# Kernel optimization log

Hardware: AMD Instinct MI355X
Metric: run time of the kernel (lower is better)

Reference implementation:

```python
import jax, jax.numpy as jnp
import numpy as np
from jax import lax

# --- STE quantizers matching the torch autograd.Functions ---
@jax.custom_vjp
def binary_quantize_w(x):
    return jnp.sign(x)

def _bqw_fwd(x):
    return jnp.sign(x), None

def _bqw_bwd(_, g):
    return (g,)  # straight-through identity

binary_quantize_w.defvjp(_bqw_fwd, _bqw_bwd)

@jax.custom_vjp
def binary_quantize_a(x):
    return jnp.sign(x)

def _bqa_fwd(x):
    return jnp.sign(x), x

def _bqa_bwd(x, g):
    return (jnp.clip(2.0 - jnp.abs(2.0 * x), a_min=0.0) * g,)

binary_quantize_a.defvjp(_bqa_fwd, _bqa_bwd)

STRIDE = 1
PAD = 1

def setup_inputs() -> dict:
    key = jax.random.key(0)
    k1, k2, k3 = jax.random.split(key, 3)
    x = jax.random.normal(k1, (32, 256, 56, 56), dtype=jnp.float32)
    M = jax.random.normal(k2, (256, 256, 3, 3), dtype=jnp.float32)
    Alpha = jax.random.uniform(k3, (256, 1, 1), dtype=jnp.float32)
    return {"x": x, "M": M, "Alpha": Alpha}

def reference(x, M, Alpha):
    bw = binary_quantize_w(M)        # (O, I, kh, kw), +/-1
    ba = binary_quantize_a(x)        # (N, C, H, W), +/-1
    out = lax.conv_general_dilated(
        ba, bw,
        window_strides=(STRIDE, STRIDE),
        padding=[(PAD, PAD), (PAD, PAD)],
        dimension_numbers=("NCHW", "OIHW", "NCHW"),
    )
    # Alpha (O,1,1) broadcasts over (N, O, H, W) trailing dims -> per-channel scale
    return out * Alpha
```

## Files before the change

kernel.cpp:

```cpp
#include <hip/hip_runtime.h>
#include <stdint.h>


typedef __attribute__((ext_vector_type(16))) float floatx16;
typedef __attribute__((ext_vector_type(8)))  int   intx8;

#define N_IMG 32
#define C_IN  256
#define O_OUT 256
#define HP 58
#define WP 58
#define GPI 3136
#define APAD_POS ((size_t)N_IMG * HP * WP)
#define APAD_BYTES (APAD_POS * C_IN)
#define TPI 13
#define AL_GRAN 1072
#define WL_GRAN 1536

__device__ __forceinline__ unsigned int sgn8(float x) {
    return x > 0.f ? 0x38u : (x < 0.f ? 0xB8u : 0u);
}

__device__ __forceinline__ void glds16(const unsigned char* g, unsigned char* l) {
    __builtin_amdgcn_global_load_lds(
        (const __attribute__((address_space(1))) unsigned int*)g,
        (__attribute__((address_space(3))) unsigned int*)l, 16, 0, 0);
}

__global__ __launch_bounds__(256) void binarize_act(
    const float* __restrict__ x, unsigned char* __restrict__ apad)
{
    int bid = blockIdx.x;
    int n = bid / HP;
    int hp = bid - n * HP;
    int tid = threadIdx.x;

    unsigned char* rowp = apad + ((size_t)(n * HP + hp) * WP) * C_IN;
    uint4 z = {0u, 0u, 0u, 0u};

    if (hp == 0 || hp == HP - 1) {
#pragma unroll
        for (int j = 0; j < 4; ++j) {
            int t = tid + 256 * j;
            if (t < WP * 16) {
                int w = t >> 4, g = t & 15;
                *(uint4*)(rowp + (size_t)w * C_IN + g * 16) = z;
            }
        }
        return;
    }
    int h = hp - 1;

    __shared__ unsigned int tile[C_IN * 15];
    __shared__ unsigned int lds2[56 * 65];

    const float* xb = x + ((size_t)n * C_IN) * GPI + h * 56;
#pragma unroll
    for (int j = 0; j < 14; ++j) {
        int t = tid + 256 * j;
        int ci = t / 14;
        int w4 = t - ci * 14;
        float4 v = *(const float4*)(xb + (size_t)ci * GPI + w4 * 4);
        tile[ci * 15 + w4] = sgn8(v.x) | (sgn8(v.y) << 8) |
                             (sgn8(v.z) << 16) | (sgn8(v.w) << 24);
    }
    __syncthreads();

#pragma unroll
    for (int j = 0; j < 14; ++j) {
        int t = tid + 256 * j;
        int wlo = t & 3;
        int cq  = (t >> 2) & 63;
        int whi = t >> 8;
        int sh = wlo * 8;
        unsigned int r = 0;
#pragma unroll
        for (int i = 0; i < 4; ++i) {
            unsigned int v = tile[(cq * 4 + i) * 15 + whi];
            r |= ((v >> sh) & 0xFFu) << (8 * i);
        }
        lds2[(whi * 4 + wlo) * 65 + cq] = r;
    }
    __syncthreads();

#pragma unroll
    for (int j = 0; j < 4; ++j) {
        int t = tid + 256 * j;
        if (t < 896) {
            int w = t >> 4, g = t & 15;
            uint4 v;
            v.x = lds2[w * 65 + g * 4 + 0];
            v.y = lds2[w * 65 + g * 4 + 1];
            v.z = lds2[w * 65 + g * 4 + 2];
            v.w = lds2[w * 65 + g * 4 + 3];
            *(uint4*)(rowp + (size_t)(w + 1) * C_IN + g * 16) = v;
        }
    }
    if (tid < 32) {
        int g = tid & 15;
        int col = (tid >> 4) * (WP - 1);
        *(uint4*)(rowp + (size_t)col * C_IN + g * 16) = z;
    }
}

__global__ __launch_bounds__(256) void pack_w(
    const float* __restrict__ M, unsigned char* __restrict__ wpk)
{
    int gid = blockIdx.x * 256 + threadIdx.x;
    int o = gid >> 6;
    int c4 = (gid & 63) << 2;
    const float* mb = M + (size_t)(o * C_IN + c4) * 9;
#pragma unroll
    for (int t = 0; t < 9; ++t) {
        unsigned int r = sgn8(mb[t]) | (sgn8(mb[9 + t]) << 8) |
                         (sgn8(mb[18 + t]) << 16) | (sgn8(mb[27 + t]) << 24);
        *(unsigned int*)(wpk + (size_t)t * 65536 + o * C_IN + c4) = r;
    }
}

__global__ __launch_bounds__(256, 2) void bconv_gemm(
    const unsigned char* __restrict__ apad,
    const unsigned char* __restrict__ wpk,
    const float* __restrict__ alpha,
    float* __restrict__ out)
{
    __shared__ __align__(16) unsigned char Al[AL_GRAN * 16];
    __shared__ __align__(16) unsigned char Wl[WL_GRAN * 16];

    const int tid = threadIdx.x;
    const int wv = tid >> 6, lane = tid & 63;
    const int l31 = lane & 31, hb = lane >> 5;

    const int bid = blockIdx.x;
    const int img = bid / 26;
    const int rem = bid - img * 26;
    const int tl = rem >> 1, ot = rem & 1;
    const int g0 = tl << 8;
    const int h0 = g0 / 56, w0 = g0 - h0 * 56;
    const int o_base = ot << 7;
    const int Q0 = (img * HP + h0) * WP + w0;

    int al_pos[5], al_sl[5];
#pragma unroll
    for (int it = 0; it < 5; ++it) {
        int s = (it < 4) ? (tid + (it << 8)) : (tid + 816);
        int pos = s >> 2, gI = s & 3;
        al_pos[it] = pos;
        al_sl[it]  = ((gI - (pos >> 1)) & 3) << 4;
    }
    int wl_off[6];
#pragma unroll
    for (int it = 0; it < 6; ++it) {
        int s = tid + (it << 8);
        int r = s >> 2, gI = s & 3;
        int kw = r >> 7, o = r & 127;
        int sl = (gI - (r >> 1)) & 3;
        wl_off[it] = kw * 65536 + o * 256 + (sl << 4);
    }

    const int o_half  = (wv >> 1) << 6;
    const int px_half = (wv & 1) << 7;

    int pos_tab[4], pxg[4];
#pragma unroll
    for (int nt = 0; nt < 4; ++nt) {
        int px = px_half + (nt << 5) + l31;
        pxg[nt] = g0 + px;
        int pxc = (pxg[nt] < GPI) ? px : (GPI - 1 - g0);
        pos_tab[nt] = pxc + 2 * ((w0 + pxc) / 56);
    }

    floatx16 acc[2][4] = {};

    for (int kh = 0; kh < 3; ++kh) {
        const int rowbase = Q0 + kh * WP;
        const int plim = (int)APAD_POS - 1 - rowbase;
        const unsigned char* asrc0 = apad + ((size_t)rowbase << 8);
        const unsigned char* wsrc0 = wpk + (size_t)(kh * 3) * 65536 + ((size_t)o_base << 8);
        for (int c0 = 0; c0 < C_IN; c0 += 64) {
            const unsigned char* asrc = asrc0 + c0;
            const unsigned char* wsrc = wsrc0 + c0;
            __syncthreads();
#pragma unroll
            for (int it = 0; it < 4; ++it) {
                int p = al_pos[it] < plim ? al_pos[it] : plim;
                glds16(asrc + ((size_t)p << 8) + al_sl[it],
                       &Al[(size_t)((it << 8) + (wv << 6)) << 4]);
            }
            {
                int p = al_pos[4] < plim ? al_pos[4] : plim;
                glds16(asrc + ((size_t)p << 8) + al_sl[4],
                       &Al[(size_t)(816 + (wv << 6)) << 4]);
            }
#pragma unroll
            for (int it = 0; it < 6; ++it)
                glds16(wsrc + wl_off[it],
                       &Wl[(size_t)((it << 8) + (wv << 6)) << 4]);
            __syncthreads();

#pragma unroll
            for (int kw = 0; kw < 3; ++kw) {
                union F { long l[4]; intx8 v; };
                F af[2];
#pragma unroll
                for (int mt = 0; mt < 2; ++mt) {
                    int r = (kw << 7) + o_half + (mt << 5) + l31;
#pragma unroll
                    for (int ks = 0; ks < 4; ++ks) {
                        int g = (r << 2) + ((ks + (r >> 1)) & 3);
                        af[mt].l[ks] = *(const long*)&Wl[(size_t)(g << 4) + (hb << 3)];
                    }
                }
#pragma unroll
                for (int nt = 0; nt < 4; ++nt) {
                    int pos = pos_tab[nt] + kw;
                    F bf;
#pragma unroll
                    for (int ks = 0; ks < 4; ++ks) {
                        int g = (pos << 2) + ((ks + (pos >> 1)) & 3);
                        bf.l[ks] = *(const long*)&Al[(size_t)(g << 4) + (hb << 3)];
                    }
#pragma unroll
                    for (int mt = 0; mt < 2; ++mt)
                        acc[mt][nt] = __builtin_amdgcn_mfma_scale_f32_32x32x64_f8f6f4(
                            af[mt].v, bf.v, acc[mt][nt],
                            0, 0,
                            0, 0x7F7F7F7F,
                            0, 0x7F7F7F7F);
                }
            }
        }
    }

#pragma unroll
    for (int mt = 0; mt < 2; ++mt) {
#pragma unroll
        for (int r = 0; r < 16; ++r) {
            int o_loc = o_half + (mt << 5) + (r & 3) + ((r >> 2) << 3) + (hb << 2);
            int o_g = o_base + o_loc;
            float a = alpha[o_g];
            float* ob = out + ((size_t)(img * O_OUT + o_g)) * GPI;
#pragma unroll
            for (int nt = 0; nt < 4; ++nt) {
                if (pxg[nt] < GPI) ob[pxg[nt]] = acc[mt][nt][r] * a;
            }
        }
    }
}

extern "C" void kernel_launch(void* const* d_in, const int* in_sizes, int n_in,
                              void* d_out, int out_size, void* d_ws, size_t ws_size,
                              hipStream_t stream) {
    const float* x     = (const float*)d_in[0];
    const float* M     = (const float*)d_in[1];
    const float* alpha = (const float*)d_in[2];
    float* out = (float*)d_out;

    unsigned char* apad = (unsigned char*)d_ws;
    unsigned char* wpk  = apad + APAD_BYTES;

    binarize_act<<<dim3(N_IMG * HP), dim3(256), 0, stream>>>(x, apad);
    pack_w<<<dim3(64), dim3(256), 0, stream>>>(M, wpk);
    bconv_gemm<<<dim3(N_IMG * TPI * 2), dim3(256), 0, stream>>>(apad, wpk, alpha, out);
}
```

Before: 274.2 us.

## Double-buffer activation tiles and load weights directly into registers

```diff
diff --git a/kernel.cpp b/kernel.cpp
--- a/kernel.cpp
+++ b/kernel.cpp
@@ -15,7 +15,6 @@
 #define APAD_BYTES (APAD_POS * C_IN)
 #define TPI 13
 #define AL_GRAN 1072
-#define WL_GRAN 1536
 
 __device__ __forceinline__ unsigned int sgn8(float x) {
     return x > 0.f ? 0x38u : (x < 0.f ? 0xB8u : 0u);
@@ -109,12 +108,14 @@
     int gid = blockIdx.x * 256 + threadIdx.x;
     int o = gid >> 6;
     int c4 = (gid & 63) << 2;
+    int cc = c4 & 63;
+    int pos = (c4 & 0xC0) + ((cc & 8) ? 32 : 0) + ((cc >> 4) << 3) + (cc & 7);
     const float* mb = M + (size_t)(o * C_IN + c4) * 9;
 #pragma unroll
     for (int t = 0; t < 9; ++t) {
         unsigned int r = sgn8(mb[t]) | (sgn8(mb[9 + t]) << 8) |
                          (sgn8(mb[18 + t]) << 16) | (sgn8(mb[27 + t]) << 24);
-        *(unsigned int*)(wpk + (size_t)t * 65536 + o * C_IN + c4) = r;
+        *(unsigned int*)(wpk + (size_t)t * 65536 + o * C_IN + pos) = r;
     }
 }
 
@@ -124,14 +125,15 @@
     const float* __restrict__ alpha,
     float* __restrict__ out)
 {
-    __shared__ __align__(16) unsigned char Al[AL_GRAN * 16];
-    __shared__ __align__(16) unsigned char Wl[WL_GRAN * 16];
+    __shared__ __align__(16) unsigned char Al[2][AL_GRAN * 16];
 
     const int tid = threadIdx.x;
     const int wv = tid >> 6, lane = tid & 63;
     const int l31 = lane & 31, hb = lane >> 5;
 
-    const int bid = blockIdx.x;
+    const int hw = blockIdx.x;
+    const int bid = (hw & 7) * 104 + (hw >> 3);
+
     const int img = bid / 26;
     const int rem = bid - img * 26;
     const int tl = rem >> 1, ot = rem & 1;
@@ -148,15 +150,6 @@
         al_pos[it] = pos;
         al_sl[it]  = ((gI - (pos >> 1)) & 3) << 4;
     }
-    int wl_off[6];
-#pragma unroll
-    for (int it = 0; it < 6; ++it) {
-        int s = tid + (it << 8);
-        int r = s >> 2, gI = s & 3;
-        int kw = r >> 7, o = r & 127;
-        int sl = (gI - (r >> 1)) & 3;
-        wl_off[it] = kw * 65536 + o * 256 + (sl << 4);
-    }
 
     const int o_half  = (wv >> 1) << 6;
     const int px_half = (wv & 1) << 7;
@@ -172,64 +165,77 @@
 
     floatx16 acc[2][4] = {};
 
-    for (int kh = 0; kh < 3; ++kh) {
-        const int rowbase = Q0 + kh * WP;
-        const int plim = (int)APAD_POS - 1 - rowbase;
-        const unsigned char* asrc0 = apad + ((size_t)rowbase << 8);
-        const unsigned char* wsrc0 = wpk + (size_t)(kh * 3) * 65536 + ((size_t)o_base << 8);
-        for (int c0 = 0; c0 < C_IN; c0 += 64) {
-            const unsigned char* asrc = asrc0 + c0;
-            const unsigned char* wsrc = wsrc0 + c0;
-            __syncthreads();
-#pragma unroll
-            for (int it = 0; it < 4; ++it) {
-                int p = al_pos[it] < plim ? al_pos[it] : plim;
-                glds16(asrc + ((size_t)p << 8) + al_sl[it],
-                       &Al[(size_t)((it << 8) + (wv << 6)) << 4]);
-            }
-            {
-                int p = al_pos[4] < plim ? al_pos[4] : plim;
-                glds16(asrc + ((size_t)p << 8) + al_sl[4],
-                       &Al[(size_t)(816 + (wv << 6)) << 4]);
-            }
-#pragma unroll
-            for (int it = 0; it < 6; ++it)
-                glds16(wsrc + wl_off[it],
-                       &Wl[(size_t)((it << 8) + (wv << 6)) << 4]);
-            __syncthreads();
-
-#pragma unroll
-            for (int kw = 0; kw < 3; ++kw) {
-                union F { long l[4]; intx8 v; };
-                F af[2];
-#pragma unroll
-                for (int mt = 0; mt < 2; ++mt) {
-                    int r = (kw << 7) + o_half + (mt << 5) + l31;
-#pragma unroll
-                    for (int ks = 0; ks < 4; ++ks) {
-                        int g = (r << 2) + ((ks + (r >> 1)) & 3);
-                        af[mt].l[ks] = *(const long*)&Wl[(size_t)(g << 4) + (hb << 3)];
-                    }
+    {
+        const int plim = (int)APAD_POS - 1 - Q0;
+        const unsigned char* asrc = apad + ((size_t)Q0 << 8);
+#pragma unroll
+        for (int it = 0; it < 5; ++it) {
+            int p = al_pos[it] < plim ? al_pos[it] : plim;
+            int dst = (it < 4) ? ((it << 8) + (wv << 6)) : (816 + (wv << 6));
+            glds16(asrc + ((size_t)p << 8) + al_sl[it], &Al[0][(size_t)dst << 4]);
+        }
+    }
+    __syncthreads();
+
+    int cur = 0;
+    for (int t = 0; t < 12; ++t) {
+        const int kh = t >> 2, c0 = (t & 3) << 6;
+
+        union WF { uint4 q[2]; intx8 v; };
+        WF wf[2][3];
+        {
+            const unsigned char* wb = wpk + (size_t)(kh * 3) * 65536 +
+                                      ((size_t)o_base << 8) + c0 + (hb << 5);
+#pragma unroll
+            for (int mt = 0; mt < 2; ++mt)
+#pragma unroll
+                for (int kw = 0; kw < 3; ++kw) {
+                    const unsigned char* p = wb + (size_t)kw * 65536 +
+                        ((size_t)(o_half + (mt << 5) + l31) << 8);
+                    wf[mt][kw].q[0] = *(const uint4*)(p);
+                    wf[mt][kw].q[1] = *(const uint4*)(p + 16);
                 }
-#pragma unroll
-                for (int nt = 0; nt < 4; ++nt) {
-                    int pos = pos_tab[nt] + kw;
-                    F bf;
-#pragma unroll
-                    for (int ks = 0; ks < 4; ++ks) {
-                        int g = (pos << 2) + ((ks + (pos >> 1)) & 3);
-                        bf.l[ks] = *(const long*)&Al[(size_t)(g << 4) + (hb << 3)];
-                    }
-#pragma unroll
-                    for (int mt = 0; mt < 2; ++mt)
-                        acc[mt][nt] = __builtin_amdgcn_mfma_scale_f32_32x32x64_f8f6f4(
-                            af[mt].v, bf.v, acc[mt][nt],
-                            0, 0,
-                            0, 0x7F7F7F7F,
-                            0, 0x7F7F7F7F);
+        }
+
+        if (t < 11) {
+            const int t1 = t + 1;
+            const int kh1 = t1 >> 2, c01 = (t1 & 3) << 6;
+            const int rowbase1 = Q0 + kh1 * WP;
+            const int plim1 = (int)APAD_POS - 1 - rowbase1;
+            const unsigned char* asrc1 = apad + (((size_t)rowbase1 << 8) + c01);
+#pragma unroll
+            for (int it = 0; it < 5; ++it) {
+                int p = al_pos[it] < plim1 ? al_pos[it] : plim1;
+                int dst = (it < 4) ? ((it << 8) + (wv << 6)) : (816 + (wv << 6));
+                glds16(asrc1 + ((size_t)p << 8) + al_sl[it],
+                       &Al[cur ^ 1][(size_t)dst << 4]);
+            }
+        }
+
+        const unsigned char* AlC = &Al[cur][0];
+#pragma unroll
+        for (int kw = 0; kw < 3; ++kw) {
+#pragma unroll
+            for (int nt = 0; nt < 4; ++nt) {
+                int pos = pos_tab[nt] + kw;
+                union F { long l[4]; intx8 v; } bf;
+#pragma unroll
+                for (int ks = 0; ks < 4; ++ks) {
+                    int g = (pos << 2) + ((ks + (pos >> 1)) & 3);
+                    bf.l[ks] = *(const long*)&AlC[(size_t)(g << 4) + (hb << 3)];
                 }
-            }
-        }
+#pragma unroll
+                for (int mt = 0; mt < 2; ++mt)
+                    acc[mt][nt] = __builtin_amdgcn_mfma_scale_f32_32x32x64_f8f6f4(
+                        wf[mt][kw].v, bf.v, acc[mt][nt],
+                        0, 0,
+                        0, 0x7F7F7F7F,
+                        0, 0x7F7F7F7F);
+            }
+        }
+
+        __syncthreads();
+        cur ^= 1;
     }
 
 #pragma unroll
```

Result: slower. 299.5 us (+9.2%).
